# Kernel optimization log

Hardware: AMD Instinct MI355X
Metric: run time of the kernel (lower is better)

## Reference

```python
import jax, jax.numpy as jnp
import numpy as np
from jax import lax

B, N, S, H = 8, 32, 512, 768   # batch, max spans, seq len, bert hidden
K, C, L = 3, 128, 64           # conv kernel height, cnn_hidden_size, num labels


def setup_inputs() -> dict:
    key = jax.random.key(0)
    ks = jax.random.split(key, 9)
    rng = np.random.default_rng(0)
    W = 16  # max span width
    starts = rng.integers(0, S - W, size=(B, N))
    widths = rng.integers(1, W + 1, size=(B, N))
    starts[0, 0], widths[0, 0] = 100, W        # force max span width = 16
    starts[0, 1], widths[0, 1] = S - W, 1      # force max prefix width = 496
    starts[0, 2], widths[0, 2] = 0, 1          # force min end = 1 -> max suffix = 511
    ends = starts + widths
    spans_dranges = jnp.asarray(np.stack([starts, ends], axis=-1), dtype=jnp.int32)
    sc = 0.02
    return {
        "tokens_emb": jax.random.normal(ks[0], (B, S, H), jnp.float32),
        "span_w": jax.random.normal(ks[1], (C, H, K), jnp.float32) * sc,
        "span_b": jax.random.normal(ks[2], (C,), jnp.float32) * sc,
        "prefix_w": jax.random.normal(ks[3], (C, H, K), jnp.float32) * sc,
        "prefix_b": jax.random.normal(ks[4], (C,), jnp.float32) * sc,
        "suffix_w": jax.random.normal(ks[5], (C, H, K), jnp.float32) * sc,
        "suffix_b": jax.random.normal(ks[6], (C,), jnp.float32) * sc,
        "fc_w": jax.random.normal(ks[7], (L, 3 * C), jnp.float32) * sc,
        "fc_b": jax.random.normal(ks[8], (L,), jnp.float32) * sc,
        "spans_dranges": spans_dranges,
        "word_seq_lengths": jnp.full((B,), S, dtype=jnp.int32),
        "max_span_width": W,
        "max_prefix_width": S - W,
        "max_suffix_width": S - 1,
    }


def _conv_pool(x, w, b):
    # x: [BN, T, H]; Conv2d(H->C, kernel (K,1)) over time + max_pool over all valid positions
    T = x.shape[1]
    if T < K:  # original pads with zeros up to kernel size
        x = jnp.pad(x, ((0, 0), (0, K - T), (0, 0)))
    y = lax.conv_general_dilated(x.transpose(0, 2, 1), w, (1,), 'VALID',
                                 dimension_numbers=('NCH', 'OIH', 'NCH'))  # [BN, C, T-K+1]
    return (y + b[None, :, None]).max(axis=2)  # pool_filter_size == full output length


def reference(tokens_emb, span_w, span_b, prefix_w, prefix_b, suffix_w, suffix_b,
              fc_w, fc_b, spans_dranges, word_seq_lengths,
              max_span_width, max_prefix_width, max_suffix_width):
    starts = spans_dranges[..., 0]  # [B,N]
    ends = spans_dranges[..., 1]

    def gather(idx, mask):
        # idx, mask: [B,N,W] -> zero-padded per-span token embeddings [B*N, W, H]
        g = jnp.take_along_axis(tokens_emb[:, None], jnp.clip(idx, 0, S - 1)[..., None], axis=2)
        return (g * mask[..., None]).reshape(B * N, -1, H)

    ar = jnp.arange(max_span_width)
    span_x = gather(starts[..., None] + ar, ar < (ends - starts)[..., None])
    arp = jnp.arange(max_prefix_width)
    prefix_x = gather(jnp.broadcast_to(arp, (B, N, max_prefix_width)), arp < starts[..., None])
    ars = jnp.arange(max_suffix_width)
    suffix_x = gather(ends[..., None] + ars,
                      ars < (word_seq_lengths[:, None, None] - ends[..., None]))

    feats = jnp.concatenate([
        _conv_pool(prefix_x, prefix_w, prefix_b),
        _conv_pool(span_x, span_w, span_b),
        _conv_pool(suffix_x, suffix_w, suffix_b),
    ], axis=-1)  # [B*N, 3C]
    probs = jax.nn.sigmoid(feats @ fc_w.T + fc_b)  # [B*N, L]
    pred_ids = (probs > 0.5).astype(jnp.int32).reshape(B, N, L)
    return probs, pred_ids
```

## Files before the change

### kernel.cpp

```cpp
#include <hip/hip_runtime.h>
#include <hip/hip_bf16.h>
#include <math.h>

#define NEG_INF (-1e30f)

typedef _Float16 half8 __attribute__((ext_vector_type(8)));
typedef _Float16 half4 __attribute__((ext_vector_type(4)));
typedef float f32x4 __attribute__((ext_vector_type(4)));
typedef float f32x16 __attribute__((ext_vector_type(16)));

__device__ __forceinline__ void load_lds16(const void* g, void* l) {
  __builtin_amdgcn_global_load_lds((const __attribute__((address_space(1))) void*)g,
                                   (__attribute__((address_space(3))) void*)l, 16, 0, 0);
}


__global__ __launch_bounds__(256) void prep(
    const float* __restrict__ tokens, const float* __restrict__ span_w,
    const float* __restrict__ prefix_w, const float* __restrict__ suffix_w,
    const float* __restrict__ fc_w, _Float16* __restrict__ A2t,
    _Float16* __restrict__ Btt, float* __restrict__ fcT) {
  __shared__ _Float16 lds[16 * 1544];
  int bid = blockIdx.x;
  int t = threadIdx.x;
  if (bid < 256) {
    int m0 = bid * 16;
#pragma unroll
    for (int r = 0; r < 12; ++r) {
      int idx4 = r * 256 + t;
      int ml = idx4 / 192;
      int hh = (idx4 % 192) * 4;
      float4 x = *(const float4*)(tokens + (size_t)m0 * 768 + (size_t)idx4 * 4);
      float xs[4] = {x.x, x.y, x.z, x.w};
#pragma unroll
      for (int i = 0; i < 4; ++i) {
        _Float16 h_ = (_Float16)xs[i];
        lds[ml * 1544 + hh + i] = h_;
        lds[ml * 1544 + 768 + hh + i] = (_Float16)((xs[i] - (float)h_) * 64.0f);
      }
    }
    __syncthreads();
#pragma unroll
    for (int rep = 0; rep < 12; ++rep) {
      int tg = rep * 16 + (t >> 4);
      int ml = t & 15;
      int g = tg & 7;
      int tt = tg >> 3;
      int p = g >> 2, ks = (g >> 1) & 1, h2 = g & 1;
      int ksrc = tt * 32 + ks * 16 + h2 * 8;
      half8 v = *(const half8*)&lds[ml * 1544 + p * 768 + ksrc];
      *(half8*)(A2t + ((size_t)tg * 4096 + m0 + ml) * 8) = v;
    }
  } else if (bid < 400) {
    int g = (bid - 256) * 256 + t;
    int ws = g / 12288;
    int r = g % 12288;
    int h8 = r >> 7, c = r & 127;
    int h0 = h8 * 8;
    const float* wsrc = (ws == 0) ? prefix_w : (ws == 1) ? span_w : suffix_w;
    const float* src = wsrc + ((size_t)c * 768 + h0) * 3;
    float wv[24];
#pragma unroll
    for (int i = 0; i < 6; ++i) *(float4*)&wv[i * 4] = *(const float4*)(src + i * 4);
    int tt = h0 >> 5, ks = (h0 >> 4) & 1, h2 = (h0 >> 3) & 1;
    int g_hi = ks * 2 + h2;
#pragma unroll
    for (int tap = 0; tap < 3; ++tap) {
      half8 hi, lo;
#pragma unroll
      for (int i = 0; i < 8; ++i) {
        float x = wv[i * 3 + tap];
        _Float16 h_ = (_Float16)x;
        hi[i] = h_;
        lo[i] = (_Float16)((x - (float)h_) * 64.0f);
      }
      int j = ws * 384 + tap * 128 + c;
      *(half8*)(Btt + ((size_t)(tt * 8 + g_hi) * 1152 + j) * 8) = hi;
      *(half8*)(Btt + ((size_t)(tt * 8 + g_hi + 4) * 1152 + j) * 8) = lo;
    }
  } else {
    int g = (bid - 400) * 256 + t;
    int i = g >> 6, c = g & 63;
    fcT[g] = fc_w[c * 384 + i];
  }
}

__global__ __launch_bounds__(384) void gemm_f16(const _Float16* __restrict__ A2t,
                                                const _Float16* __restrict__ Btt,
                                                float* __restrict__ Ct) {
  __shared__ _Float16 S[2][10240];
  const int bm = blockIdx.x * 64;
  const int bj = blockIdx.y * 96;
  const int tid = threadIdx.x;
  const int w = tid >> 6;
  const int lane = tid & 63;
  const int nu = (w < 2) ? 4 : 3;
  const int ub = (w < 2) ? (w * 4) : (8 + 3 * (w - 2));
  const _Float16* su[4];
  size_t ts[4];
  int du[4];
#pragma unroll
  for (int i = 0; i < 4; ++i) {
    int u = ub + ((i < nu) ? i : 0);
    du[i] = u * 512;
    if (u < 8) {
      su[i] = A2t + ((size_t)u * 4096 + bm + lane) * 8;
      ts[i] = 262144;
    } else {
      int fr = (u - 8) * 64 + lane;
      int g = fr / 96, jr = fr % 96;
      su[i] = Btt + ((size_t)g * 1152 + bj + jr) * 8;
      ts[i] = 73728;
    }
  }
  const _Float16* su0 = su[0];
  const _Float16* su1 = su[1];
  const _Float16* su2 = su[2];
  const _Float16* su3 = su[3];
  const size_t ts0 = ts[0], ts1 = ts[1], ts2 = ts[2], ts3 = ts[3];
  const int du0 = du[0], du1 = du[1], du2 = du[2], du3 = du[3];
#define STAGE(buf, t)                                              \
  do {                                                             \
    load_lds16(su0 + (size_t)(t) * ts0, &S[(buf)][du0]);           \
    load_lds16(su1 + (size_t)(t) * ts1, &S[(buf)][du1]);           \
    load_lds16(su2 + (size_t)(t) * ts2, &S[(buf)][du2]);           \
    if (w < 2) load_lds16(su3 + (size_t)(t) * ts3, &S[(buf)][du3]); \
  } while (0)
#define WAIT_NU()                                                  \
  do {                                                             \
    if (w < 2)                                                     \
      asm volatile("s_waitcnt vmcnt(4)" ::: "memory");             \
    else                                                           \
      asm volatile("s_waitcnt vmcnt(3)" ::: "memory");             \
  } while (0)
  const int ln31 = lane & 31;
  const int hi32 = lane >> 5;
  const int wm = w & 1;
  const int wn = w >> 1;
  const int aoff = (wm * 32 + ln31) * 8;
  const int boff = 4096 + (wn * 32 + ln31) * 8;
  f32x16 aa, ab;
#pragma unroll
  for (int q = 0; q < 16; ++q) {
    aa[q] = 0.f;
    ab[q] = 0.f;
  }
  STAGE(0, 0);
  STAGE(1, 1);
  WAIT_NU();
  asm volatile("s_barrier" ::: "memory");

  for (int t = 0; t < 24; ++t) {
    const int cur = t & 1;
    half8 a0[2], a1[2], b0[2], b1[2];
#pragma unroll
    for (int ks = 0; ks < 2; ++ks) {
      const int gb = ks * 2 + hi32;
      a0[ks] = *(const half8*)&S[cur][gb * 512 + aoff];
      a1[ks] = *(const half8*)&S[cur][(gb + 4) * 512 + aoff];
      b0[ks] = *(const half8*)&S[cur][boff + gb * 768];
      b1[ks] = *(const half8*)&S[cur][boff + (gb + 4) * 768];
    }
    asm volatile("s_waitcnt lgkmcnt(0)" ::: "memory");
    __builtin_amdgcn_sched_barrier(0);
    asm volatile("s_barrier" ::: "memory");
    if (t + 2 < 24) STAGE(cur, t + 2);
    __builtin_amdgcn_s_setprio(1);
#pragma unroll
    for (int ks = 0; ks < 2; ++ks) {
      aa = __builtin_amdgcn_mfma_f32_32x32x16_f16(a0[ks], b0[ks], aa, 0, 0, 0);
      ab = __builtin_amdgcn_mfma_f32_32x32x16_f16(a1[ks], b0[ks], ab, 0, 0, 0);
      ab = __builtin_amdgcn_mfma_f32_32x32x16_f16(a0[ks], b1[ks], ab, 0, 0, 0);
    }
    __builtin_amdgcn_s_setprio(0);
    if (t < 23) {
      if (t < 22) {
        WAIT_NU();
      } else {
        asm volatile("s_waitcnt vmcnt(0)" ::: "memory");
      }
      asm volatile("s_barrier" ::: "memory");
    }
  }
#undef STAGE
#undef WAIT_NU
  const int n_out = bj + wn * 32 + ln31;
  float* cp = Ct + (size_t)n_out * 4096 + bm + wm * 32 + 4 * hi32;
#pragma unroll
  for (int r = 0; r < 4; ++r) {
    f32x4 v;
#pragma unroll
    for (int q = 0; q < 4; ++q) v[q] = aa[4 * r + q] + 0.015625f * ab[4 * r + q];
    *(f32x4*)(cp + 8 * r) = v;
  }
}

__global__ __launch_bounds__(256) void scan_kernel(const float* __restrict__ Ct,
                                                   const int* __restrict__ wsl,
                                                   float* __restrict__ PM2,
                                                   float* __restrict__ SM2) {
  int pair = blockIdx.x * 4 + (threadIdx.x >> 6);
  int b = pair >> 7;
  int c = pair & 127;
  int lane = threadIdx.x & 63;
  int mb = b * 512;
  int t0 = lane * 8;
  const float* p0 = Ct + (size_t)(0 + c) * 4096 + mb;
  const float* p1 = Ct + (size_t)(128 + c) * 4096 + mb;
  const float* p2 = Ct + (size_t)(256 + c) * 4096 + mb;
  float v[8];
#pragma unroll
  for (int i = 0; i < 8; i++) {
    int t = t0 + i;
    v[i] = (t < 494) ? (p0[t] + p1[t + 1] + p2[t + 2]) : NEG_INF;
  }
#pragma unroll
  for (int i = 1; i < 8; i++) v[i] = fmaxf(v[i], v[i - 1]);
  float x = v[7];
#pragma unroll
  for (int d = 1; d < 64; d <<= 1) {
    float y = __shfl_up(x, d);
    if (lane >= d) x = fmaxf(x, y);
  }
  float excl = __shfl_up(x, 1);
  if (lane == 0) excl = NEG_INF;
  float* pm = PM2 + (size_t)pair * 512;
#pragma unroll
  for (int i = 0; i < 8; i++) {
    int t = t0 + i;
    if (t < 494) pm[t] = fmaxf(v[i], excl);
  }
  const float* s0 = Ct + (size_t)(768 + c) * 4096 + mb;
  const float* s1 = Ct + (size_t)(896 + c) * 4096 + mb;
  const float* s2 = Ct + (size_t)(1024 + c) * 4096 + mb;
  int qmax = wsl[b] - 3;
  if (qmax > 509) qmax = 509;
  float u[8];
#pragma unroll
  for (int i = 0; i < 8; i++) {
    int q = t0 + i;
    u[i] = (q <= qmax) ? (s0[q] + s1[q + 1] + s2[q + 2]) : NEG_INF;
  }
#pragma unroll
  for (int i = 6; i >= 0; i--) u[i] = fmaxf(u[i], u[i + 1]);
  float xr = u[0];
#pragma unroll
  for (int d = 1; d < 64; d <<= 1) {
    float y = __shfl_down(xr, d);
    if (lane < 64 - d) xr = fmaxf(xr, y);
  }
  float exclr = __shfl_down(xr, 1);
  if (lane == 63) exclr = NEG_INF;
  float* sm = SM2 + (size_t)pair * 512;
#pragma unroll
  for (int i = 0; i < 8; i++) sm[t0 + i] = fmaxf(u[i], exclr);
}

__global__ __launch_bounds__(128) void span_kernel(
    const float* __restrict__ Ct, const float* __restrict__ PM2,
    const float* __restrict__ SM2, const float* __restrict__ prefix_b,
    const float* __restrict__ span_b, const float* __restrict__ suffix_b,
    const float* __restrict__ fcT, const float* __restrict__ fc_b,
    const int* __restrict__ spans, const int* __restrict__ wsl,
    float* __restrict__ out) {
  __shared__ float sfeat[384];
  __shared__ float part[64];
  int sp = blockIdx.x;
  int b = sp >> 5;
  int c = threadIdx.x;
  int s = spans[sp * 2], e = spans[sp * 2 + 1];
  int Lb = wsl[b];
  int mb = b * 512;
  {
    const float* t0p = Ct + (size_t)c * 4096 + mb;
    const float* t1p = Ct + (size_t)(128 + c) * 4096 + mb;
    float m = NEG_INF;
    if (s >= 3) m = fmaxf(m, PM2[(size_t)(b * 128 + c) * 512 + s - 3]);
    if (s >= 2 && s <= 495) m = fmaxf(m, t0p[s - 2] + t1p[s - 1]);
    if (s >= 1 && s <= 494) m = fmaxf(m, t0p[s - 1]);
    if (s <= 493) m = fmaxf(m, 0.0f);
    sfeat[c] = m + prefix_b[c];
  }
  {
    const float* u0 = Ct + (size_t)(384 + c) * 4096 + mb;
    const float* u1 = Ct + (size_t)(512 + c) * 4096 + mb;
    const float* u2 = Ct + (size_t)(640 + c) * 4096 + mb;
    int w = e - s;
    float m = NEG_INF;
    for (int p = 0; p + 2 < w; ++p)
      m = fmaxf(m, u0[s + p] + u1[s + p + 1] + u2[s + p + 2]);
    if (w >= 2 && w <= 15) m = fmaxf(m, u0[s + w - 2] + u1[s + w - 1]);
    if (w <= 14) m = fmaxf(m, u0[s + w - 1]);
    if (w <= 13) m = fmaxf(m, 0.0f);
    sfeat[128 + c] = m + span_b[c];
  }
  {
    const float* x0 = Ct + (size_t)(768 + c) * 4096 + mb;
    const float* x1 = Ct + (size_t)(896 + c) * 4096 + mb;
    float m = NEG_INF;
    if (e <= Lb - 3) m = fmaxf(m, SM2[(size_t)(b * 128 + c) * 512 + e]);
    if (Lb - 2 - e >= 0 && Lb - 2 - e <= 508)
      m = fmaxf(m, x0[Lb - 2] + x1[Lb - 1]);
    if (Lb - 1 - e >= 0 && Lb - 1 - e <= 508) m = fmaxf(m, x0[Lb - 1]);
    if (Lb - e <= 508) m = fmaxf(m, 0.0f);
    sfeat[256 + c] = m + suffix_b[c];
  }
  __syncthreads();
  {
    int cc = threadIdx.x & 63;
    int half = threadIdx.x >> 6;
    float acc2 = 0.0f;
    const float* fp = fcT + (size_t)(half * 192) * 64 + cc;
    const float* sf = sfeat + half * 192;
#pragma unroll 8
    for (int i = 0; i < 192; ++i) acc2 = fmaf(sf[i], fp[(size_t)i * 64], acc2);
    if (half) part[cc] = acc2;
    __syncthreads();
    if (!half) {
      float a = acc2 + part[cc] + fc_b[cc];
      float pr = 1.0f / (1.0f + expf(-a));
      out[sp * 64 + cc] = pr;
      out[16384 + sp * 64 + cc] = (pr > 0.5f) ? 1.0f : 0.0f;
    }
  }
}

extern "C" void kernel_launch(void* const* d_in, const int* in_sizes, int n_in,
                              void* d_out, int out_size, void* d_ws,
                              size_t ws_size, hipStream_t stream) {
  const float* tokens = (const float*)d_in[0];
  const float* span_w = (const float*)d_in[1];
  const float* span_b = (const float*)d_in[2];
  const float* prefix_w = (const float*)d_in[3];
  const float* prefix_b = (const float*)d_in[4];
  const float* suffix_w = (const float*)d_in[5];
  const float* suffix_b = (const float*)d_in[6];
  const float* fc_w = (const float*)d_in[7];
  const float* fc_b = (const float*)d_in[8];
  const int* spans = (const int*)d_in[9];
  const int* wsl = (const int*)d_in[10];
  float* out = (float*)d_out;

  char* ws = (char*)d_ws;
  float* Ct = (float*)ws;
  _Float16* A2t = (_Float16*)(ws + 18874368);
  _Float16* Btt = (_Float16*)(ws + 31457280);
  float* PM2 = (float*)(ws + 34996224);
  float* SM2 = (float*)(ws + 37093376);
  float* fcT = (float*)(ws + 39190528);

  hipLaunchKernelGGL(prep, dim3(496), dim3(256), 0, stream, tokens, span_w,
                     prefix_w, suffix_w, fc_w, A2t, Btt, fcT);
  hipLaunchKernelGGL(gemm_f16, dim3(64, 12), dim3(384), 0, stream, A2t, Btt, Ct);
  hipLaunchKernelGGL(scan_kernel, dim3(256), dim3(256), 0, stream, Ct, wsl,
                     PM2, SM2);
  hipLaunchKernelGGL(span_kernel, dim3(256), dim3(128), 0, stream, Ct, PM2,
                     SM2, prefix_b, span_b, suffix_b, fcT, fc_b, spans, wsl,
                     out);
}
```

Measured before the change: 143.2 us.

## Load GEMM B operand directly into registers, shrink LDS to A tiles only

The B (weight) tile is no longer staged through LDS. Each wave now loads its B fragments straight from global memory into registers with inline global_load_dwordx4, double-buffered across iterations, and LDS holds only the A tiles. This cuts LDS traffic and footprint (down to 16 KB per block) and adds a launch-bounds occupancy hint of 5 blocks per SM, aiming to raise occupancy and drop one round of LDS reads per iteration. In exchange, B data is read redundantly from global or L2 by the waves that share it, and the hand-written vmcnt waits must match the exact load counts.

Result: slower. 148.4 us (+3.6%).

```diff
diff --git a/kernel.cpp b/kernel.cpp
--- a/kernel.cpp
+++ b/kernel.cpp
@@ -85,105 +85,98 @@
   }
 }
 
-__global__ __launch_bounds__(384) void gemm_f16(const _Float16* __restrict__ A2t,
-                                                const _Float16* __restrict__ Btt,
-                                                float* __restrict__ Ct) {
-  __shared__ _Float16 S[2][10240];
+__global__ __launch_bounds__(384, 5) void gemm_f16(const _Float16* __restrict__ A2t,
+                                                   const _Float16* __restrict__ Btt,
+                                                   float* __restrict__ Ct) {
+  __shared__ _Float16 S[2][4096];
   const int bm = blockIdx.x * 64;
   const int bj = blockIdx.y * 96;
   const int tid = threadIdx.x;
   const int w = tid >> 6;
   const int lane = tid & 63;
-  const int nu = (w < 2) ? 4 : 3;
-  const int ub = (w < 2) ? (w * 4) : (8 + 3 * (w - 2));
-  const _Float16* su[4];
-  size_t ts[4];
-  int du[4];
-#pragma unroll
-  for (int i = 0; i < 4; ++i) {
-    int u = ub + ((i < nu) ? i : 0);
-    du[i] = u * 512;
-    if (u < 8) {
-      su[i] = A2t + ((size_t)u * 4096 + bm + lane) * 8;
-      ts[i] = 262144;
-    } else {
-      int fr = (u - 8) * 64 + lane;
-      int g = fr / 96, jr = fr % 96;
-      su[i] = Btt + ((size_t)g * 1152 + bj + jr) * 8;
-      ts[i] = 73728;
-    }
-  }
-  const _Float16* su0 = su[0];
-  const _Float16* su1 = su[1];
-  const _Float16* su2 = su[2];
-  const _Float16* su3 = su[3];
-  const size_t ts0 = ts[0], ts1 = ts[1], ts2 = ts[2], ts3 = ts[3];
-  const int du0 = du[0], du1 = du[1], du2 = du[2], du3 = du[3];
+  const int uA = (w < 2) ? (w * 2) : (w + 2);
+  const _Float16* sA0 = A2t + ((size_t)uA * 4096 + bm + lane) * 8;
+  const _Float16* sA1 = A2t + ((size_t)(uA + 1) * 4096 + bm + lane) * 8;
+  const int dA0 = uA * 512;
+  const int dA1 = (uA + 1) * 512;
+  const size_t tsA = 262144;
 #define STAGE(buf, t)                                              \
   do {                                                             \
-    load_lds16(su0 + (size_t)(t) * ts0, &S[(buf)][du0]);           \
-    load_lds16(su1 + (size_t)(t) * ts1, &S[(buf)][du1]);           \
-    load_lds16(su2 + (size_t)(t) * ts2, &S[(buf)][du2]);           \
-    if (w < 2) load_lds16(su3 + (size_t)(t) * ts3, &S[(buf)][du3]); \
-  } while (0)
-#define WAIT_NU()                                                  \
-  do {                                                             \
-    if (w < 2)                                                     \
-      asm volatile("s_waitcnt vmcnt(4)" ::: "memory");             \
-    else                                                           \
-      asm volatile("s_waitcnt vmcnt(3)" ::: "memory");             \
+    load_lds16(sA0 + (size_t)(t) * tsA, &S[(buf)][dA0]);           \
+    if (w < 2) load_lds16(sA1 + (size_t)(t) * tsA, &S[(buf)][dA1]); \
   } while (0)
   const int ln31 = lane & 31;
   const int hi32 = lane >> 5;
   const int wm = w & 1;
   const int wn = w >> 1;
+  uint64_t ba0 = (uint64_t)(Btt + ((size_t)hi32 * 1152 + bj + wn * 32 + ln31) * 8);
+  uint64_t ba1 = ba0 + 2ull * 1152 * 16;
+  uint64_t ba2 = ba0 + 4ull * 1152 * 16;
+  uint64_t ba3 = ba0 + 6ull * 1152 * 16;
+  const uint64_t BSTR = 147456ull;
+  f32x4 P0, P1, P2, P3, Q0, Q1, Q2, Q3;
+#define LOADB(R0, R1, R2, R3)                                                  \
+  do {                                                                         \
+    asm volatile("global_load_dwordx4 %0, %1, off" : "=&v"(R0) : "v"(ba0));    \
+    asm volatile("global_load_dwordx4 %0, %1, off" : "=&v"(R1) : "v"(ba1));    \
+    asm volatile("global_load_dwordx4 %0, %1, off" : "=&v"(R2) : "v"(ba2));    \
+    asm volatile("global_load_dwordx4 %0, %1, off" : "=&v"(R3) : "v"(ba3));    \
+    ba0 += BSTR; ba1 += BSTR; ba2 += BSTR; ba3 += BSTR;                        \
+  } while (0)
   const int aoff = (wm * 32 + ln31) * 8;
-  const int boff = 4096 + (wn * 32 + ln31) * 8;
   f32x16 aa, ab;
 #pragma unroll
   for (int q = 0; q < 16; ++q) {
     aa[q] = 0.f;
     ab[q] = 0.f;
   }
+  LOADB(P0, P1, P2, P3);
   STAGE(0, 0);
   STAGE(1, 1);
-  WAIT_NU();
+  if (w < 2)
+    asm volatile("s_waitcnt vmcnt(2)" ::: "memory");
+  else
+    asm volatile("s_waitcnt vmcnt(1)" ::: "memory");
   asm volatile("s_barrier" ::: "memory");
 
-  for (int t = 0; t < 24; ++t) {
-    const int cur = t & 1;
-    half8 a0[2], a1[2], b0[2], b1[2];
-#pragma unroll
-    for (int ks = 0; ks < 2; ++ks) {
-      const int gb = ks * 2 + hi32;
-      a0[ks] = *(const half8*)&S[cur][gb * 512 + aoff];
-      a1[ks] = *(const half8*)&S[cur][(gb + 4) * 512 + aoff];
-      b0[ks] = *(const half8*)&S[cur][boff + gb * 768];
-      b1[ks] = *(const half8*)&S[cur][boff + (gb + 4) * 768];
-    }
-    asm volatile("s_waitcnt lgkmcnt(0)" ::: "memory");
-    __builtin_amdgcn_sched_barrier(0);
-    asm volatile("s_barrier" ::: "memory");
-    if (t + 2 < 24) STAGE(cur, t + 2);
-    __builtin_amdgcn_s_setprio(1);
-#pragma unroll
-    for (int ks = 0; ks < 2; ++ks) {
-      aa = __builtin_amdgcn_mfma_f32_32x32x16_f16(a0[ks], b0[ks], aa, 0, 0, 0);
-      ab = __builtin_amdgcn_mfma_f32_32x32x16_f16(a1[ks], b0[ks], ab, 0, 0, 0);
-      ab = __builtin_amdgcn_mfma_f32_32x32x16_f16(a0[ks], b1[ks], ab, 0, 0, 0);
-    }
-    __builtin_amdgcn_s_setprio(0);
-    if (t < 23) {
-      if (t < 22) {
-        WAIT_NU();
-      } else {
-        asm volatile("s_waitcnt vmcnt(0)" ::: "memory");
-      }
-      asm volatile("s_barrier" ::: "memory");
-    }
-  }
+#define ITER(t, cur, B0c, B1c, B2c, B3c, B0n, B1n, B2n, B3n)                   \
+  {                                                                            \
+    half8 a0k0 = *(const half8*)&S[cur][(0 + hi32) * 512 + aoff];              \
+    half8 a1k0 = *(const half8*)&S[cur][(4 + hi32) * 512 + aoff];              \
+    half8 a0k1 = *(const half8*)&S[cur][(2 + hi32) * 512 + aoff];              \
+    half8 a1k1 = *(const half8*)&S[cur][(6 + hi32) * 512 + aoff];              \
+    if ((t) + 1 < 24) LOADB(B0n, B1n, B2n, B3n);                               \
+    asm volatile("s_waitcnt lgkmcnt(0)" ::: "memory");                         \
+    if ((t) < 23)                                                              \
+      asm volatile("s_waitcnt vmcnt(4)" ::: "memory");                         \
+    else                                                                       \
+      asm volatile("s_waitcnt vmcnt(0)" ::: "memory");                         \
+    __builtin_amdgcn_sched_barrier(0);                                         \
+    if ((t) < 23) asm volatile("s_barrier" ::: "memory");                      \
+    if ((t) + 2 < 24) STAGE(cur, (t) + 2);                                     \
+    __builtin_amdgcn_s_setprio(1);                                             \
+    aa = __builtin_amdgcn_mfma_f32_32x32x16_f16(                               \
+        a0k0, __builtin_bit_cast(half8, B0c), aa, 0, 0, 0);                    \
+    ab = __builtin_amdgcn_mfma_f32_32x32x16_f16(                               \
+        a1k0, __builtin_bit_cast(half8, B0c), ab, 0, 0, 0);                    \
+    ab = __builtin_amdgcn_mfma_f32_32x32x16_f16(                               \
+        a0k0, __builtin_bit_cast(half8, B2c), ab, 0, 0, 0);                    \
+    aa = __builtin_amdgcn_mfma_f32_32x32x16_f16(                               \
+        a0k1, __builtin_bit_cast(half8, B1c), aa, 0, 0, 0);                    \
+    ab = __builtin_amdgcn_mfma_f32_32x32x16_f16(                               \
+        a1k1, __builtin_bit_cast(half8, B1c), ab, 0, 0, 0);                    \
+    ab = __builtin_amdgcn_mfma_f32_32x32x16_f16(                               \
+        a0k1, __builtin_bit_cast(half8, B3c), ab, 0, 0, 0);                    \
+    __builtin_amdgcn_s_setprio(0);                                             \
+  }
+
+  for (int tt = 0; tt < 12; ++tt) {
+    ITER(2 * tt, 0, P0, P1, P2, P3, Q0, Q1, Q2, Q3);
+    ITER(2 * tt + 1, 1, Q0, Q1, Q2, Q3, P0, P1, P2, P3);
+  }
+#undef ITER
+#undef LOADB
 #undef STAGE
-#undef WAIT_NU
   const int n_out = bj + wn * 32 + ln31;
   float* cp = Ct + (size_t)n_out * 4096 + bm + wm * 32 + 4 * hi32;
 #pragma unroll
```
